# Kernel optimization log

Hardware: AMD Instinct MI355X
Metric: run time of the kernel (lower is better)

Reference implementation:

```python
import jax, jax.numpy as jnp
import numpy as np

N_FILTRATIONS = 24
TEMPERATURE = 0.15
H1_WEIGHT = 0.5
LAMBDA_TOPO = 0.1


def setup_inputs() -> dict:
    key = jax.random.key(0)
    embeddings = jax.random.normal(key, (4096, 512), dtype=jnp.float32)
    return {"embeddings": embeddings, "step": 0}


def _landscape_loss(embeddings):
    N = embeddings.shape[0]
    emb = embeddings.astype(jnp.float32)
    # pairwise euclidean distances (torch.cdist p=2), safe sqrt for grad at 0
    sq = jnp.sum(emb * emb, axis=1)
    d2 = sq[:, None] + sq[None, :] - 2.0 * (emb @ emb.T)
    d2 = jnp.maximum(d2, 0.0)
    pos = d2 > 1e-12
    dist = jnp.where(pos, jnp.sqrt(jnp.where(pos, d2, 1.0)), 0.0)
    eye = jnp.eye(N, dtype=jnp.float32)
    dist = dist + eye * 1e9  # [N, N], diag pushed to 'infinity'
    off = dist < 1e8
    # thresholds come from .item() in torch -> no grad through them
    d_min = jax.lax.stop_gradient(jnp.min(jnp.where(off, dist, jnp.inf)))
    d_max = jax.lax.stop_gradient(
        jnp.maximum(jnp.max(jnp.where(off, dist, -jnp.inf)), d_min + 1e-4))
    thresholds = jnp.linspace(d_min, d_max, N_FILTRATIONS)

    one_minus_eye = 1.0 - eye

    def step_fn(carry, thresh):
        adj = jax.nn.sigmoid((thresh - dist) / TEMPERATURE) * one_minus_eye
        deg = jnp.clip(jnp.sum(adj, axis=-1), 1e-6, None)
        n_isolated = jnp.sum((deg < 0.5).astype(jnp.float32))  # H0 proxy
        n_edges_soft = jnp.sum(adj) / 2.0
        n_excess = jax.nn.relu(n_edges_soft - (N - 1)) / N  # H1 proxy
        return carry, (n_isolated, n_excess)

    _, (h0, h1) = jax.lax.scan(step_fn, None, thresholds)
    h0_loss = jnp.mean(h0[-8:])
    h1_loss = jnp.mean(h1)
    total = h0_loss + H1_WEIGHT * h1_loss
    return total * LAMBDA_TOPO


def reference(embeddings, step) -> jnp.ndarray:
    # warmup_steps = 0, so the warmup skip branch never triggers;
    # N == max_points, so no subsampling.
    return _landscape_loss(embeddings)
```

## Files before the change

kernel.cpp:

```cpp
#include <hip/hip_runtime.h>
#include <stdint.h>

typedef float f32x4 __attribute__((ext_vector_type(4)));
typedef short s16x8 __attribute__((ext_vector_type(8)));
typedef unsigned short us4 __attribute__((ext_vector_type(4)));

#define NPTS 4096
#define DDIM 512
#define NF   24
#define NBLK 32
#define NB   2048

#define OFF_SQ  4194304
#define OFF_MM  4210688
#define OFF_DEG 4210752
#define OFF_D   4603968
#define OFF_H   38158400ULL
#define WS_A    54935616ULL

typedef __attribute__((address_space(1))) void gvoid;
typedef __attribute__((address_space(3))) void svoid;
#define GLD16(gp, lp) __builtin_amdgcn_global_load_lds((gvoid*)(gp), (svoid*)(lp), 16, 0, 0)

static __device__ __forceinline__ ushort f2h(float x) {
    _Float16 h = (_Float16)x;
    return __builtin_bit_cast(unsigned short, h);
}
static __device__ __forceinline__ float h2f(ushort u) {
    return (float)__builtin_bit_cast(_Float16, u);
}

__global__ __launch_bounds__(256) void k_init(float* __restrict__ deg,
                                              unsigned* __restrict__ mm) {
    int i = blockIdx.x * 256 + threadIdx.x;
    if (i < NPTS * NF) deg[i] = 0.0f;
    if (i == 0) { mm[0] = 0x7F7FFFFFu; mm[1] = 0u; }
}

__global__ __launch_bounds__(256) void k_convert(const float* __restrict__ in,
                                                 ushort* __restrict__ Eb,
                                                 float* __restrict__ sq,
                                                 float* __restrict__ acc32,
                                                 unsigned* __restrict__ mm) {
    if (blockIdx.x == 0) {
        if (threadIdx.x < 32) acc32[threadIdx.x] = 0.0f;
        else if (threadIdx.x == 32) mm[0] = 0x7F7FFFFFu;
        else if (threadIdx.x == 33) mm[1] = 0u;
    }
    const int w = threadIdx.x >> 6, lane = threadIdx.x & 63;
    const int row = blockIdx.x * 4 + w;
    const float* src = in + (size_t)row * DDIM + lane * 8;
    float4 a = ((const float4*)src)[0];
    float4 b = ((const float4*)src)[1];
    float v[8] = {a.x, a.y, a.z, a.w, b.x, b.y, b.z, b.w};
    unsigned u[8];
    float ss = 0.0f;
#pragma unroll
    for (int i = 0; i < 8; ++i) {
        ss += v[i] * v[i];
        unsigned bits = __float_as_uint(v[i]);
        u[i] = (bits + 0x7FFFu + ((bits >> 16) & 1u)) >> 16;
    }
    uint4 pk;
    pk.x = u[0] | (u[1] << 16);
    pk.y = u[2] | (u[3] << 16);
    pk.z = u[4] | (u[5] << 16);
    pk.w = u[6] | (u[7] << 16);
    *(uint4*)(Eb + (size_t)row * DDIM + lane * 8) = pk;
#pragma unroll
    for (int s = 1; s < 64; s <<= 1) ss += __shfl_xor(ss, s);
    if (lane == 0) sq[row] = ss;
}

__global__ __launch_bounds__(256) void k_gram_v3(const ushort* __restrict__ Eb,
                                                 const float* __restrict__ sq,
                                                 unsigned* __restrict__ mm,
                                                 ushort* __restrict__ D2h) {
    __shared__ __align__(16) ushort SM[17408];
    __shared__ float sqr[128], sqc[128], red[8];
    char* SMb = (char*)SM;
    const int tid = threadIdx.x;
    const int w = tid >> 6, lane = tid & 63, g = lane >> 4, l15 = lane & 15;
    const int wr = w >> 1, wc = w & 1;

    const int bid = (blockIdx.x & 7) * 128 + (blockIdx.x >> 3);
    const int rb = bid >> 5, cb = bid & 31;

    if (tid < 128) sqr[tid] = sq[rb * 128 + tid];
    else           sqc[tid - 128] = sq[cb * 128 + (tid - 128)];

    f32x4 acc[4][4];
#pragma unroll
    for (int i = 0; i < 4; ++i)
#pragma unroll
        for (int j = 0; j < 4; ++j) acc[i][j] = (f32x4){0.f, 0.f, 0.f, 0.f};

    const int lrow = lane >> 2, lch = lane & 3;

#define STAGE(buf, kk)                                                          \
    {                                                                           \
        const int k0_ = (kk) * 32;                                              \
        _Pragma("unroll")                                                       \
        for (int i_ = 0; i_ < 2; ++i_) {                                        \
            const int r_  = w * 32 + i_ * 16 + lrow;                            \
            const int ch_ = lch ^ ((r_ >> 1) & 3);                              \
            GLD16(Eb + (size_t)(rb * 128 + r_) * DDIM + k0_ + ch_ * 8,          \
                  SMb + (buf) * 8192 + (w * 32 + i_ * 16) * 64);                \
            GLD16(Eb + (size_t)(cb * 128 + r_) * DDIM + k0_ + ch_ * 8,          \
                  SMb + 16384 + (buf) * 8192 + (w * 32 + i_ * 16) * 64);        \
        }                                                                       \
    }

    STAGE(0, 0);
    int cur = 0;
#pragma unroll 1
    for (int kk = 0; kk < 16; ++kk) {
        __syncthreads();
        if (kk < 15) STAGE(cur ^ 1, kk + 1);
        s16x8 rf[4], cf[4];
#pragma unroll
        for (int i = 0; i < 4; ++i) {
            const int r = wr * 64 + i * 16 + l15;
            rf[i] = *(const s16x8*)(SMb + cur * 8192 + r * 64 + ((g ^ ((r >> 1) & 3)) * 16));
        }
#pragma unroll
        for (int j = 0; j < 4; ++j) {
            const int r = wc * 64 + j * 16 + l15;
            cf[j] = *(const s16x8*)(SMb + 16384 + cur * 8192 + r * 64 + ((g ^ ((r >> 1) & 3)) * 16));
        }
#pragma unroll
        for (int i = 0; i < 4; ++i)
#pragma unroll
            for (int j = 0; j < 4; ++j)
                acc[i][j] = __builtin_amdgcn_mfma_f32_16x16x32_bf16(cf[j], rf[i], acc[i][j], 0, 0, 0);
        cur ^= 1;
    }
    __syncthreads();

    ushort* T = SM;
    float mn = 3.4e38f, mx = 0.0f;
#pragma unroll
    for (int i = 0; i < 4; ++i) {
        const int lr = wr * 64 + i * 16 + l15;
        const int trow = rb * 128 + lr;
        const float srv = sqr[lr];
#pragma unroll
        for (int j = 0; j < 4; ++j) {
            const int c0 = wc * 64 + j * 16 + g * 4;
            const int tc0 = cb * 128 + c0;
            ushort h[4];
#pragma unroll
            for (int m = 0; m < 4; ++m) {
                float d2 = srv + sqc[c0 + m] - 2.0f * acc[i][j][m];
                d2 = fmaxf(d2, 0.0f);
                bool diag = (tc0 + m == trow);
                mn = diag ? mn : fminf(mn, d2);
                mx = diag ? mx : fmaxf(mx, d2);
                h[m] = f2h(diag ? 6.0e4f : d2);
            }
            us4 pk4 = {h[0], h[1], h[2], h[3]};
            *(us4*)(T + lr * 136 + c0) = pk4;
        }
    }
#pragma unroll
    for (int s = 1; s < 64; s <<= 1) {
        mn = fminf(mn, __shfl_xor(mn, s));
        mx = fmaxf(mx, __shfl_xor(mx, s));
    }
    if (lane == 0) { red[w] = mn; red[4 + w] = mx; }
    __syncthreads();
    if (tid == 0) {
        mn = fminf(fminf(red[0], red[1]), fminf(red[2], red[3]));
        mx = fmaxf(fmaxf(red[4], red[5]), fmaxf(red[6], red[7]));
        atomicMin(&mm[0], __float_as_uint(mn));
        atomicMax(&mm[1], __float_as_uint(mx));
    }
#pragma unroll
    for (int j = 0; j < 8; ++j) {
        const int c = j * 256 + tid;
        const int row = c >> 4, col8 = (c & 15) * 8;
        uint4 v = *(const uint4*)(T + row * 136 + col8);
        *(uint4*)(D2h + (size_t)(rb * 128 + row) * NPTS + cb * 128 + col8) = v;
    }
}

__global__ __launch_bounds__(256) void k_hist(const ushort* __restrict__ D2h,
                                              const unsigned* __restrict__ mm,
                                              ushort* __restrict__ H) {
    __shared__ unsigned hist[2][NB + 8];
    const int tid = threadIdx.x;
    const int row = blockIdx.x;
    const int cp = (tid >> 6) & 1;
    for (int i = tid; i < 2 * (NB + 8); i += 256) ((unsigned*)hist)[i] = 0u;
    const float d2min = __uint_as_float(mm[0]);
    const float d2max = __uint_as_float(mm[1]);
    const float sc = (float)NB / fmaxf(d2max - d2min, 1e-6f);
    __syncthreads();
    const uint4* Dv = (const uint4*)(D2h + (size_t)row * NPTS);
#pragma unroll
    for (int c = 0; c < 2; ++c) {
        uint4 pk = Dv[c * 256 + tid];
        unsigned pw[4] = {pk.x, pk.y, pk.z, pk.w};
#pragma unroll
        for (int i = 0; i < 4; ++i) {
            float a = h2f((ushort)(pw[i] & 0xFFFFu));
            float b = h2f((ushort)(pw[i] >> 16));
            if (a < 3.0e4f) {
                int ba = (int)fminf(fmaxf((a - d2min) * sc, 0.0f), (float)(NB - 1));
                atomicAdd(&hist[cp][ba], 1u);
            }
            if (b < 3.0e4f) {
                int bb = (int)fminf(fmaxf((b - d2min) * sc, 0.0f), (float)(NB - 1));
                atomicAdd(&hist[cp][bb], 1u);
            }
        }
    }
    __syncthreads();
    unsigned o[4];
#pragma unroll
    for (int p = 0; p < 4; ++p) {
        const int b0 = tid * 8 + 2 * p, b1 = b0 + 1;
        unsigned lo = hist[0][b0] + hist[1][b0];
        unsigned hi = hist[0][b1] + hist[1][b1];
        o[p] = (lo & 0xFFFFu) | (hi << 16);
    }
    *(uint4*)(H + (size_t)row * NB + tid * 8) = *(uint4*)o;
}

__global__ __launch_bounds__(512) void k_dot(const ushort* __restrict__ H,
                                             const unsigned* __restrict__ mm,
                                             float* __restrict__ acc32) {
    __shared__ float Wl[4][NB];
    __shared__ float degb[8][NF];
    const int tid = threadIdx.x;
    const int wid = tid >> 6, lane = tid & 63;
    const int row = blockIdx.x * 8 + wid;

    const float d2min = __uint_as_float(mm[0]);
    const float d2max = __uint_as_float(mm[1]);
    const float bw    = fmaxf(d2max - d2min, 1e-6f) / (float)NB;
    const float d_min = d2min > 1e-12f ? sqrtf(d2min) : 0.0f;
    const float d_mx  = d2max > 1e-12f ? sqrtf(d2max) : 0.0f;
    const float d_max = fmaxf(d_mx, d_min + 1e-4f);
    const float stp   = (d_max - d_min) / 23.0f;
    const float S2L   = (1.0f / 0.15f) * 1.44269504f;
    const float Ds2   = stp * S2L;
    const float R     = exp2f(-Ds2);
    const float LIM   = 1073741824.0f;

    float hv[32];
    const ushort* Hr = H + (size_t)row * NB;
#pragma unroll
    for (int j = 0; j < 8; ++j) {
        uint2 pk = *(const uint2*)(Hr + j * 256 + lane * 4);
        hv[j * 4 + 0] = (float)(pk.x & 0xFFFFu);
        hv[j * 4 + 1] = (float)(pk.x >> 16);
        hv[j * 4 + 2] = (float)(pk.y & 0xFFFFu);
        hv[j * 4 + 3] = (float)(pk.y >> 16);
    }

    float e4[4];
#pragma unroll
    for (int q = 0; q < 4; ++q) {
        const int b = tid * 4 + q;
        const float d2c = d2min + ((float)b + 0.5f) * bw;
        const float db = sqrtf(fmaxf(d2c, 0.0f));
        e4[q] = exp2f(fminf((db - d_min) * S2L, 125.0f));
    }

#pragma unroll 1
    for (int ph = 0; ph < 6; ++ph) {
        __syncthreads();
#pragma unroll
        for (int k = 0; k < 4; ++k) {
            f32x4 sg;
#pragma unroll
            for (int q = 0; q < 4; ++q) {
                sg[q] = __builtin_amdgcn_rcpf(1.0f + fminf(e4[q], LIM));
                e4[q] *= R;
            }
            *(f32x4*)(&Wl[k][tid * 4]) = sg;
        }
        __syncthreads();
        float dacc[4];
#pragma unroll
        for (int k = 0; k < 4; ++k) {
            const float* Wr = &Wl[k][0];
            float s = 0.0f;
#pragma unroll
            for (int j = 0; j < 8; ++j) {
                const f32x4 wv = *(const f32x4*)(Wr + j * 256 + lane * 4);
                s += hv[j*4+0]*wv[0] + hv[j*4+1]*wv[1] + hv[j*4+2]*wv[2] + hv[j*4+3]*wv[3];
            }
            dacc[k] = s;
        }
#pragma unroll
        for (int k = 0; k < 4; ++k)
#pragma unroll
            for (int o = 1; o < 64; o <<= 1) dacc[k] += __shfl_xor(dacc[k], o);
        if (lane == 0) {
#pragma unroll
            for (int k = 0; k < 4; ++k) degb[wid][ph * 4 + k] = dacc[k];
        }
    }
    __syncthreads();
    if (tid < NF) {
        float s = 0.0f;
#pragma unroll
        for (int r = 0; r < 8; ++r) s += degb[r][tid];
        atomicAdd(&acc32[tid], s);
    } else if (tid < 32) {
        const int k = 16 + (tid - NF);
        float c = 0.0f;
#pragma unroll
        for (int r = 0; r < 8; ++r) c += (degb[r][k] < 0.5f) ? 1.0f : 0.0f;
        atomicAdd(&acc32[tid], c);
    }
}

__global__ __launch_bounds__(64) void k_final2(const float* __restrict__ acc32,
                                               float* __restrict__ out) {
    if (threadIdx.x == 0) {
        float h1 = 0.0f;
#pragma unroll
        for (int k = 0; k < NF; ++k)
            h1 += fmaxf(acc32[k] * 0.5f - (float)(NPTS - 1), 0.0f) * (1.0f / (float)NPTS);
        float h0 = 0.0f;
#pragma unroll
        for (int k = 0; k < 8; ++k) h0 += acc32[NF + k];
        out[0] = (h0 * 0.125f + 0.5f * (h1 * (1.0f / 24.0f))) * 0.1f;
    }
}

__device__ __forceinline__ void gram_tile(const ushort* __restrict__ Eb, int rb, int cb,
                                          ushort* As, ushort* Bs, f32x4 acc[2][8]) {
    const int tid = threadIdx.x;
    const int w = tid >> 6, lane = tid & 63, g = lane >> 4, l15 = lane & 15;
#pragma unroll 1
    for (int kk = 0; kk < DDIM / 32; ++kk) {
        const int k0 = kk * 32;
        __syncthreads();
#pragma unroll
        for (int it = 0; it < 2; ++it) {
            int li  = it * 256 + tid;
            int row = li >> 2, ch = li & 3;
            uint4 va = *(const uint4*)(Eb + (size_t)(rb * 128 + row) * DDIM + k0 + ch * 8);
            uint4 vb = *(const uint4*)(Eb + (size_t)(cb * 128 + row) * DDIM + k0 + ch * 8);
            *(uint4*)(As + row * 32 + ch * 8) = va;
            *(uint4*)(Bs + row * 32 + ch * 8) = vb;
        }
        __syncthreads();
        s16x8 rf0 = *(const s16x8*)(As + (w * 32 + 0 * 16 + l15) * 32 + g * 8);
        s16x8 rf1 = *(const s16x8*)(As + (w * 32 + 1 * 16 + l15) * 32 + g * 8);
#pragma unroll
        for (int bj = 0; bj < 8; ++bj) {
            s16x8 cf = *(const s16x8*)(Bs + (bj * 16 + l15) * 32 + g * 8);
            acc[0][bj] = __builtin_amdgcn_mfma_f32_16x16x32_bf16(cf, rf0, acc[0][bj], 0, 0, 0);
            acc[1][bj] = __builtin_amdgcn_mfma_f32_16x16x32_bf16(cf, rf1, acc[1][bj], 0, 0, 0);
        }
    }
}

__global__ __launch_bounds__(256) void k_minmax(const ushort* __restrict__ Eb,
                                                const float* __restrict__ sq,
                                                unsigned* __restrict__ mm) {
    const int rb = blockIdx.y, cb = blockIdx.x;
    if (cb < rb) return;
    __shared__ ushort As[128 * 32], Bs[128 * 32];
    __shared__ float sqr[128], sqc[128];
    __shared__ float red[8];
    const int tid = threadIdx.x;
    if (tid < 128) sqr[tid] = sq[rb * 128 + tid];
    else           sqc[tid - 128] = sq[cb * 128 + (tid - 128)];
    f32x4 acc[2][8];
#pragma unroll
    for (int bi = 0; bi < 2; ++bi)
#pragma unroll
        for (int bj = 0; bj < 8; ++bj) acc[bi][bj] = (f32x4){0.f, 0.f, 0.f, 0.f};
    gram_tile(Eb, rb, cb, As, Bs, acc);
    const int w = tid >> 6, lane = tid & 63, g = lane >> 4, l15 = lane & 15;
    const float sr0 = sqr[w * 32 + l15], sr1 = sqr[w * 32 + 16 + l15];
    float mn = 3.4e38f, mx = 0.0f;
#pragma unroll
    for (int bi = 0; bi < 2; ++bi)
#pragma unroll
        for (int bj = 0; bj < 8; ++bj)
#pragma unroll
            for (int m = 0; m < 4; ++m) {
                int tr = w * 32 + bi * 16 + l15;
                int tc = bj * 16 + g * 4 + m;
                float d2 = (bi ? sr1 : sr0) + sqc[tc] - 2.0f * acc[bi][bj][m];
                d2 = fmaxf(d2, 0.0f);
                bool diag = (rb == cb) && (tr == tc);
                mn = diag ? mn : fminf(mn, d2);
                mx = diag ? mx : fmaxf(mx, d2);
            }
#pragma unroll
    for (int s = 1; s < 64; s <<= 1) {
        mn = fminf(mn, __shfl_xor(mn, s));
        mx = fmaxf(mx, __shfl_xor(mx, s));
    }
    if (lane == 0) { red[w] = mn; red[4 + w] = mx; }
    __syncthreads();
    if (tid == 0) {
        mn = fminf(fminf(red[0], red[1]), fminf(red[2], red[3]));
        mx = fmaxf(fmaxf(red[4], red[5]), fmaxf(red[6], red[7]));
        atomicMin(&mm[0], __float_as_uint(mn));
        atomicMax(&mm[1], __float_as_uint(mx));
    }
}

__global__ __launch_bounds__(256) void k_accum2(const ushort* __restrict__ Eb,
                                                const float* __restrict__ sq,
                                                const unsigned* __restrict__ mm,
                                                float* __restrict__ deg) {
    const int rb = blockIdx.y, cb = blockIdx.x;
    __shared__ ushort As[128 * 32], Bs[128 * 32];
    __shared__ float sqr[128], sqc[128];
    __shared__ float degr[128][NF];
    const int tid = threadIdx.x;
    if (tid < 128) sqr[tid] = sq[rb * 128 + tid];
    else           sqc[tid - 128] = sq[cb * 128 + (tid - 128)];
    for (int i = tid; i < 128 * NF; i += 256) ((float*)degr)[i] = 0.0f;
    f32x4 acc[2][8];
#pragma unroll
    for (int bi = 0; bi < 2; ++bi)
#pragma unroll
        for (int bj = 0; bj < 8; ++bj) acc[bi][bj] = (f32x4){0.f, 0.f, 0.f, 0.f};
    gram_tile(Eb, rb, cb, As, Bs, acc);
    const int w = tid >> 6, lane = tid & 63, g = lane >> 4, l15 = lane & 15;

    const float dmin2 = __uint_as_float(mm[0]);
    const float dmax2 = __uint_as_float(mm[1]);
    const float d_min = dmin2 > 1e-12f ? sqrtf(dmin2) : 0.0f;
    const float d_mx  = dmax2 > 1e-12f ? sqrtf(dmax2) : 0.0f;
    const float d_max = fmaxf(d_mx, d_min + 1e-4f);
    const float stp   = (d_max - d_min) / 23.0f;
    const float S2L   = (1.0f / 0.15f) * 1.44269504f;
    const float Ds2   = stp * S2L;
    const float R     = exp2f(-Ds2);
    const float LIM   = 1073741824.0f;
    const float ECAP  = 125.0f;

    const float sr0 = sqr[w * 32 + l15], sr1 = sqr[w * 32 + 16 + l15];
    f32x4 ee[2][8];
#pragma unroll
    for (int bi = 0; bi < 2; ++bi)
#pragma unroll
        for (int bj = 0; bj < 8; ++bj)
#pragma unroll
            for (int m = 0; m < 4; ++m) {
                int tr = w * 32 + bi * 16 + l15;
                int tc = bj * 16 + g * 4 + m;
                float d2 = (bi ? sr1 : sr0) + sqc[tc] - 2.0f * acc[bi][bj][m];
                d2 = fmaxf(d2, 0.0f);
                float d = d2 > 1e-12f ? sqrtf(d2) : 0.0f;
                if (rb == cb && tr == tc) d = 1e9f;
                ee[bi][bj][m] = exp2f(fminf((d - d_min) * S2L, ECAP));
            }

#pragma unroll 1
    for (int t = 0; t < NF; ++t) {
        float rs0 = 0.0f, rs1 = 0.0f;
#pragma unroll
        for (int bj = 0; bj < 8; ++bj) {
            {
                f32x4 q = ee[0][bj];
                float A  = 1.0f + fminf(q.x, LIM), B  = 1.0f + fminf(q.y, LIM);
                float Cq = 1.0f + fminf(q.z, LIM), Dq = 1.0f + fminf(q.w, LIM);
                float sAB = A + B,  sCD = Cq + Dq;
                float pAB = A * B,  pCD = Cq * Dq;
                rs0 += (sAB * pCD + sCD * pAB) * __builtin_amdgcn_rcpf(pAB * pCD);
                ee[0][bj] = q * R;
            }
            {
                f32x4 q = ee[1][bj];
                float A  = 1.0f + fminf(q.x, LIM), B  = 1.0f + fminf(q.y, LIM);
                float Cq = 1.0f + fminf(q.z, LIM), Dq = 1.0f + fminf(q.w, LIM);
                float sAB = A + B,  sCD = Cq + Dq;
                float pAB = A * B,  pCD = Cq * Dq;
                rs1 += (sAB * pCD + sCD * pAB) * __builtin_amdgcn_rcpf(pAB * pCD);
                ee[1][bj] = q * R;
            }
        }
        rs0 += __shfl_xor(rs0, 16); rs0 += __shfl_xor(rs0, 32);
        rs1 += __shfl_xor(rs1, 16); rs1 += __shfl_xor(rs1, 32);
        if (g == 0) {
            degr[w * 32 + l15][t]      += rs0;
            degr[w * 32 + 16 + l15][t] += rs1;
        }
    }
    __syncthreads();
    for (int i = tid; i < 128 * NF; i += 256) {
        int r = i / NF, t = i % NF;
        atomicAdd(&deg[(size_t)(rb * 128 + r) * NF + t], degr[r][t]);
    }
}

__global__ __launch_bounds__(256) void k_final(const float* __restrict__ deg,
                                               float* __restrict__ out) {
    const int tid = threadIdx.x;
    float s[NF], cnt[8];
#pragma unroll
    for (int t = 0; t < NF; ++t) s[t] = 0.0f;
#pragma unroll
    for (int k = 0; k < 8; ++k) cnt[k] = 0.0f;
    for (int i = tid; i < NPTS; i += 256) {
        const float* row = deg + (size_t)i * NF;
#pragma unroll
        for (int t = 0; t < NF; ++t) {
            float v = row[t];
            s[t] += v;
            if (t >= 16) cnt[t - 16] += (v < 0.5f) ? 1.0f : 0.0f;
        }
    }
#pragma unroll
    for (int t = 0; t < NF; ++t)
#pragma unroll
        for (int o = 1; o < 64; o <<= 1) s[t] += __shfl_xor(s[t], o);
#pragma unroll
    for (int k = 0; k < 8; ++k)
#pragma unroll
        for (int o = 1; o < 64; o <<= 1) cnt[k] += __shfl_xor(cnt[k], o);
    __shared__ float red[4][32];
    const int w = tid >> 6, lane = tid & 63;
    if (lane == 0) {
#pragma unroll
        for (int t = 0; t < NF; ++t) red[w][t] = s[t];
#pragma unroll
        for (int k = 0; k < 8; ++k) red[w][NF + k] = cnt[k];
    }
    __syncthreads();
    if (tid == 0) {
        float h0 = 0.0f, h1 = 0.0f;
#pragma unroll
        for (int t = 0; t < NF; ++t) {
            float S = red[0][t] + red[1][t] + red[2][t] + red[3][t];
            float edges = S * 0.5f;
            h1 += fmaxf(edges - (float)(NPTS - 1), 0.0f) / (float)NPTS;
        }
#pragma unroll
        for (int k = 0; k < 8; ++k)
            h0 += red[0][NF + k] + red[1][NF + k] + red[2][NF + k] + red[3][NF + k];
        h0 *= (1.0f / 8.0f);
        h1 *= (1.0f / 24.0f);
        out[0] = (h0 + 0.5f * h1) * 0.1f;
    }
}

extern "C" void kernel_launch(void* const* d_in, const int* in_sizes, int n_in,
                              void* d_out, int out_size, void* d_ws, size_t ws_size,
                              hipStream_t stream) {
    (void)in_sizes; (void)n_in; (void)out_size;
    const float* emb = (const float*)d_in[0];
    uint8_t* ws = (uint8_t*)d_ws;
    ushort*   Eb  = (ushort*)(ws);
    float*    sqv = (float*)(ws + OFF_SQ);
    unsigned* mm  = (unsigned*)(ws + OFF_MM);
    float*    deg = (float*)(ws + OFF_DEG);
    ushort*   D2h = (ushort*)(ws + OFF_D);
    ushort*   H   = (ushort*)(ws + OFF_H);
    float*    out = (float*)d_out;
    const bool bigws = (ws_size >= WS_A);

    if (bigws) {
        k_convert<<<dim3(NPTS / 4),    dim3(256), 0, stream>>>(emb, Eb, sqv, deg, mm);
        k_gram_v3<<<dim3(NBLK * NBLK), dim3(256), 0, stream>>>(Eb, sqv, mm, D2h);
        k_hist   <<<dim3(NPTS),        dim3(256), 0, stream>>>(D2h, mm, H);
        k_dot    <<<dim3(NPTS / 8),    dim3(512), 0, stream>>>(H, mm, deg);
        k_final2 <<<dim3(1),           dim3(64),  0, stream>>>(deg, out);
    } else {
        k_init   <<<dim3(384),      dim3(256), 0, stream>>>(deg, mm);
        k_convert<<<dim3(NPTS / 4), dim3(256), 0, stream>>>(emb, Eb, sqv, deg, mm);
        k_minmax <<<dim3(32, 32),   dim3(256), 0, stream>>>(Eb, sqv, mm);
        k_accum2 <<<dim3(32, 32),   dim3(256), 0, stream>>>(Eb, sqv, mm, deg);
        k_final  <<<dim3(1),        dim3(256), 0, stream>>>(deg, out);
    }
}
```

Baseline: 90.57 us.

## Exploit Gram symmetry with upper-triangle tiles and mirrored writes; batch histogram rows

```diff
diff --git a/kernel.cpp b/kernel.cpp
--- a/kernel.cpp
+++ b/kernel.cpp
@@ -72,10 +72,10 @@
     if (lane == 0) sq[row] = ss;
 }
 
-__global__ __launch_bounds__(256) void k_gram_v3(const ushort* __restrict__ Eb,
-                                                 const float* __restrict__ sq,
-                                                 unsigned* __restrict__ mm,
-                                                 ushort* __restrict__ D2h) {
+__global__ __launch_bounds__(256) void k_gram_v3u(const ushort* __restrict__ Eb,
+                                                  const float* __restrict__ sq,
+                                                  unsigned* __restrict__ mm,
+                                                  ushort* __restrict__ D2h) {
     __shared__ __align__(16) ushort SM[17408];
     __shared__ float sqr[128], sqc[128], red[8];
     char* SMb = (char*)SM;
@@ -83,8 +83,9 @@
     const int w = tid >> 6, lane = tid & 63, g = lane >> 4, l15 = lane & 15;
     const int wr = w >> 1, wc = w & 1;
 
-    const int bid = (blockIdx.x & 7) * 128 + (blockIdx.x >> 3);
-    const int rb = bid >> 5, cb = bid & 31;
+    int bid = blockIdx.x, rb = 0, pre = 0;
+    while (pre + (NBLK - rb) <= bid) { pre += NBLK - rb; ++rb; }
+    const int cb = rb + (bid - pre);
 
     if (tid < 128) sqr[tid] = sq[rb * 128 + tid];
     else           sqc[tid - 128] = sq[cb * 128 + (tid - 128)];
@@ -182,24 +183,40 @@
         uint4 v = *(const uint4*)(T + row * 136 + col8);
         *(uint4*)(D2h + (size_t)(rb * 128 + row) * NPTS + cb * 128 + col8) = v;
     }
-}
-
-__global__ __launch_bounds__(256) void k_hist(const ushort* __restrict__ D2h,
-                                              const unsigned* __restrict__ mm,
-                                              ushort* __restrict__ H) {
-    __shared__ unsigned hist[2][NB + 8];
-    const int tid = threadIdx.x;
-    const int row = blockIdx.x;
-    const int cp = (tid >> 6) & 1;
-    for (int i = tid; i < 2 * (NB + 8); i += 256) ((unsigned*)hist)[i] = 0u;
+    if (rb != cb) {
+        const int ocol = tid >> 1, oh = tid & 1;
+#pragma unroll
+        for (int j2 = 0; j2 < 8; ++j2) {
+            unsigned pw[4];
+#pragma unroll
+            for (int p = 0; p < 4; ++p) {
+                unsigned lo = T[(oh * 64 + j2 * 8 + 2 * p) * 136 + ocol];
+                unsigned hi = T[(oh * 64 + j2 * 8 + 2 * p + 1) * 136 + ocol];
+                pw[p] = lo | (hi << 16);
+            }
+            *(uint4*)(D2h + (size_t)(cb * 128 + ocol) * NPTS + rb * 128 + oh * 64 + j2 * 8) =
+                *(uint4*)pw;
+        }
+    }
+}
+
+__global__ __launch_bounds__(256) void k_hist4(const ushort* __restrict__ D2h,
+                                               const unsigned* __restrict__ mm,
+                                               ushort* __restrict__ H) {
+    __shared__ unsigned Hs[4][NB + 4];
+    const int tid = threadIdx.x, w = tid >> 6, lane = tid & 63;
+    const int row0 = blockIdx.x * 4;
+    const int row = row0 + w;
+    for (int i = tid; i < 4 * (NB + 4); i += 256) ((unsigned*)Hs)[i] = 0u;
     const float d2min = __uint_as_float(mm[0]);
     const float d2max = __uint_as_float(mm[1]);
     const float sc = (float)NB / fmaxf(d2max - d2min, 1e-6f);
     __syncthreads();
     const uint4* Dv = (const uint4*)(D2h + (size_t)row * NPTS);
-#pragma unroll
-    for (int c = 0; c < 2; ++c) {
-        uint4 pk = Dv[c * 256 + tid];
+    unsigned* hr = Hs[w];
+#pragma unroll
+    for (int it = 0; it < 8; ++it) {
+        uint4 pk = Dv[it * 64 + lane];
         unsigned pw[4] = {pk.x, pk.y, pk.z, pk.w};
 #pragma unroll
         for (int i = 0; i < 4; ++i) {
@@ -207,24 +224,21 @@
             float b = h2f((ushort)(pw[i] >> 16));
             if (a < 3.0e4f) {
                 int ba = (int)fminf(fmaxf((a - d2min) * sc, 0.0f), (float)(NB - 1));
-                atomicAdd(&hist[cp][ba], 1u);
+                atomicAdd(&hr[ba], 1u);
             }
             if (b < 3.0e4f) {
                 int bb = (int)fminf(fmaxf((b - d2min) * sc, 0.0f), (float)(NB - 1));
-                atomicAdd(&hist[cp][bb], 1u);
-            }
-        }
-    }
-    __syncthreads();
-    unsigned o[4];
-#pragma unroll
-    for (int p = 0; p < 4; ++p) {
-        const int b0 = tid * 8 + 2 * p, b1 = b0 + 1;
-        unsigned lo = hist[0][b0] + hist[1][b0];
-        unsigned hi = hist[0][b1] + hist[1][b1];
-        o[p] = (lo & 0xFFFFu) | (hi << 16);
-    }
-    *(uint4*)(H + (size_t)row * NB + tid * 8) = *(uint4*)o;
+                atomicAdd(&hr[bb], 1u);
+            }
+        }
+    }
+    __syncthreads();
+    unsigned* Ho = (unsigned*)(H + (size_t)row0 * NB);
+    for (int i = tid; i < 4 * (NB / 2); i += 256) {
+        const int r = i >> 10, pw_ = i & 1023;
+        unsigned lo = Hs[r][2 * pw_], hi = Hs[r][2 * pw_ + 1];
+        Ho[r * (NB / 2) + pw_] = (lo & 0xFFFFu) | (hi << 16);
+    }
 }
 
 __global__ __launch_bounds__(512) void k_dot(const ushort* __restrict__ H,
@@ -564,11 +578,11 @@
     const bool bigws = (ws_size >= WS_A);
 
     if (bigws) {
-        k_convert<<<dim3(NPTS / 4),    dim3(256), 0, stream>>>(emb, Eb, sqv, deg, mm);
-        k_gram_v3<<<dim3(NBLK * NBLK), dim3(256), 0, stream>>>(Eb, sqv, mm, D2h);
-        k_hist   <<<dim3(NPTS),        dim3(256), 0, stream>>>(D2h, mm, H);
-        k_dot    <<<dim3(NPTS / 8),    dim3(512), 0, stream>>>(H, mm, deg);
-        k_final2 <<<dim3(1),           dim3(64),  0, stream>>>(deg, out);
+        k_convert <<<dim3(NPTS / 4),              dim3(256), 0, stream>>>(emb, Eb, sqv, deg, mm);
+        k_gram_v3u<<<dim3(NBLK * (NBLK + 1) / 2), dim3(256), 0, stream>>>(Eb, sqv, mm, D2h);
+        k_hist4   <<<dim3(NPTS / 4),              dim3(256), 0, stream>>>(D2h, mm, H);
+        k_dot     <<<dim3(NPTS / 8),              dim3(512), 0, stream>>>(H, mm, deg);
+        k_final2  <<<dim3(1),                     dim3(64),  0, stream>>>(deg, out);
     } else {
         k_init   <<<dim3(384),      dim3(256), 0, stream>>>(deg, mm);
         k_convert<<<dim3(NPTS / 4), dim3(256), 0, stream>>>(emb, Eb, sqv, deg, mm);
```

Result: faster. 85.55 us (-5.5%).
